# Performance work log

Hardware: AMD Instinct MI355X
Metric: run time of the kernel (lower is better)

The kernel has to match this reference:

```python
import jax, jax.numpy as jnp
import numpy as np

N = 100000
E = 3200000
F_IN = 256
HID = 128


def _dconv_k1(x_cat, w, b):
    # torch_geometric_temporal DConv with K=1:
    # H = X @ W[0,0] + X @ W[1,0] + b   (no graph propagation for K=1)
    return x_cat @ (w[0, 0] + w[1, 0]) + b


def _dcrnn_cell(x, h, wz, bz, wr, br, wh, bh):
    xh = jnp.concatenate([x, h], axis=1)
    z = jax.nn.sigmoid(_dconv_k1(xh, wz, bz))
    r = jax.nn.sigmoid(_dconv_k1(xh, wr, br))
    xrh = jnp.concatenate([x, r * h], axis=1)
    h_tilde = jnp.tanh(_dconv_k1(xrh, wh, bh))
    return z * h + (1.0 - z) * h_tilde


def setup_inputs() -> dict:
    key = jax.random.key(0)
    ks = jax.random.split(key, 16)

    def gw(k, shape):
        fan_in = shape[-2]
        return jax.random.normal(k, shape, dtype=jnp.float32) / np.sqrt(fan_in)

    inp = {
        "x": jax.random.normal(ks[0], (N, F_IN), dtype=jnp.float32),
        "edge_index": jax.random.randint(ks[1], (2, E), 0, N, dtype=jnp.int64 if jax.config.jax_enable_x64 else jnp.int32),
        "edge_weight": jax.random.uniform(ks[2], (E,), dtype=jnp.float32),
        "w_z1": gw(ks[3], (2, 1, F_IN + HID, HID)), "b_z1": jnp.zeros((HID,), jnp.float32),
        "w_r1": gw(ks[4], (2, 1, F_IN + HID, HID)), "b_r1": jnp.zeros((HID,), jnp.float32),
        "w_h1": gw(ks[5], (2, 1, F_IN + HID, HID)), "b_h1": jnp.zeros((HID,), jnp.float32),
        "w_z2": gw(ks[6], (2, 1, HID + HID // 2, HID // 2)), "b_z2": jnp.zeros((HID // 2,), jnp.float32),
        "w_r2": gw(ks[7], (2, 1, HID + HID // 2, HID // 2)), "b_r2": jnp.zeros((HID // 2,), jnp.float32),
        "w_h2": gw(ks[8], (2, 1, HID + HID // 2, HID // 2)), "b_h2": jnp.zeros((HID // 2,), jnp.float32),
        "w_lin1": gw(ks[9], (HID // 2, 16)), "b_lin1": jnp.zeros((16,), jnp.float32),
        "w_lin2": gw(ks[10], (16, 1)), "b_lin2": jnp.zeros((1,), jnp.float32),
    }
    return inp


def reference(x, edge_index, edge_weight,
              w_z1, b_z1, w_r1, b_r1, w_h1, b_h1,
              w_z2, b_z2, w_r2, b_r2, w_h2, b_h2,
              w_lin1, b_lin1, w_lin2, b_lin2):
    # edge_index / edge_weight are unused in the K=1 DConv math (faithful to tgt source).
    h0 = jnp.zeros((x.shape[0], w_z1.shape[-1]), x.dtype)
    h = _dcrnn_cell(x, h0, w_z1, b_z1, w_r1, b_r1, w_h1, b_h1)
    h = jax.nn.relu(h)
    h0b = jnp.zeros((x.shape[0], w_z2.shape[-1]), x.dtype)
    h = _dcrnn_cell(h, h0b, w_z2, b_z2, w_r2, b_r2, w_h2, b_h2)
    h = jax.nn.relu(h)
    # Dropout(0.2) is identity at inference
    h = jax.nn.relu(h @ w_lin1 + b_lin1)
    return h @ w_lin2 + b_lin2
```

## Files before the change

kernel.cpp:

```cpp
#include <hip/hip_runtime.h>

typedef _Float16 f16;
typedef _Float16 f16x4 __attribute__((ext_vector_type(4)));
typedef _Float16 f16x8 __attribute__((ext_vector_type(8)));
typedef float    f32x4 __attribute__((ext_vector_type(4)));

#define N_ROWS 100000
#define RT 1563
#define TPB 256
#define LSX 264
#define LSH1 136
#define LSH2 72

#define W1F_OFF 0
#define W1F_BYTES (256 * 256 * 2)
#define W2F_OFF W1F_BYTES

#define ARENA 33792
#define H1S 0
#define H2S 17408

__global__ void prep_w(const float* __restrict__ wz1, const float* __restrict__ wh1,
                       const float* __restrict__ wz2, const float* __restrict__ wh2,
                       f16* __restrict__ W1F, f16* __restrict__ W2F) {
    const int b = blockIdx.x, tid = threadIdx.x;
    if (b < 32) {
        int idx = b * 256 + tid;
        int l = idx & 63, itm = idx >> 6;
        int it = itm & 7, M = itm >> 3;
        int ln = l & 15, q = l >> 4;
        int col = M * 16 + ln;
        int k0 = it * 32 + q * 8;
        const float* w = (col < 128) ? wz1 : wh1;
        int cc = col & 127;
        f16x8 v;
#pragma unroll
        for (int j = 0; j < 8; ++j) {
            int k = k0 + j;
            v[j] = (f16)(w[k * 128 + cc] + w[384 * 128 + k * 128 + cc]);
        }
        *(f16x8*)&W1F[idx * 8] = v;
    } else {
        int idx = (b - 32) * 256 + tid;
        if (idx >= 2048) return;
        int l = idx & 63, tkc = idx >> 6;
        int kc = tkc & 3, t = tkc >> 2;
        int ln = l & 15, q = l >> 4;
        int col = (t < 4) ? (16 * t + ln) : (64 + 16 * (t - 4) + ln);
        int k0 = kc * 32 + q * 8;
        const float* w = (col < 64) ? wz2 : wh2;
        int cc = col & 63;
        f16x8 v;
#pragma unroll
        for (int j = 0; j < 8; ++j) {
            int k = k0 + j;
            v[j] = (f16)(w[k * 64 + cc] + w[192 * 64 + k * 64 + cc]);
        }
        *(f16x8*)&W2F[idx * 8] = v;
    }
}

__device__ __forceinline__ float gate(float zp, float hp) {
    float e2h = __expf(2.0f * fminf(hp, 15.0f));
    float ez  = __expf(zp);
    float r   = __builtin_amdgcn_rcpf((e2h + 1.0f) * (1.0f + ez));
    return fmaxf((e2h - 1.0f) * r, 0.0f);
}

__global__ __launch_bounds__(TPB, 3) void fused(
    const float* __restrict__ x,
    const f16* __restrict__ W1F, const f16* __restrict__ W2F,
    const float* __restrict__ bz1, const float* __restrict__ bh1,
    const float* __restrict__ bz2, const float* __restrict__ bh2,
    const float* __restrict__ wl1, const float* __restrict__ bl1,
    const float* __restrict__ wl2, const float* __restrict__ bl2,
    float* __restrict__ out)
{
    __shared__ __align__(16) char arena[ARENA];
    const int tid = threadIdx.x, lane = tid & 63, wave = tid >> 6;
    const int ln = lane & 15, quad = lane >> 4;
    const int r0 = blockIdx.x * 64;

    const int xr = tid >> 2, xcg = tid & 3;
    int gxr = r0 + xr; if (gxr >= N_ROWS) gxr = N_ROWS - 1;
    const float* xp = x + (size_t)gxr * 256 + (xcg << 3);

    f16* Xs = (f16*)arena;

    const f16* wb0 = W1F + (size_t)wave * 4096 + (size_t)lane * 8;

    f32x4 acc[4][4];
#pragma unroll
    for (int a = 0; a < 4; ++a)
#pragma unroll
        for (int b = 0; b < 4; ++b) acc[a][b] = (f32x4){0.f, 0.f, 0.f, 0.f};

    f32x4 pa = __builtin_nontemporal_load((const f32x4*)(xp));
    f32x4 pb = __builtin_nontemporal_load((const f32x4*)(xp + 4));
    f16x8 afc[4], afn[4];
#pragma unroll
    for (int mi = 0; mi < 4; ++mi)
        afc[mi] = *(const f16x8*)(wb0 + mi * 16384);

#pragma unroll
    for (int s = 0; s < 8; ++s) {
        *(f16x8*)&Xs[xr * LSX + s * 32 + (xcg << 3)] =
            (f16x8){(f16)pa[0],(f16)pa[1],(f16)pa[2],(f16)pa[3],
                    (f16)pb[0],(f16)pb[1],(f16)pb[2],(f16)pb[3]};
        asm volatile("s_waitcnt lgkmcnt(0)" ::: "memory");
        __builtin_amdgcn_s_barrier();
        asm volatile("" ::: "memory");
        if (s < 7) {
            pa = __builtin_nontemporal_load((const f32x4*)(xp + (s + 1) * 32));
            pb = __builtin_nontemporal_load((const f32x4*)(xp + (s + 1) * 32 + 4));
#pragma unroll
            for (int mi = 0; mi < 4; ++mi)
                afn[mi] = *(const f16x8*)(wb0 + mi * 16384 + (s + 1) * 512);
        }
        f16x8 bf[4];
#pragma unroll
        for (int nt = 0; nt < 4; ++nt)
            bf[nt] = *(const f16x8*)&Xs[(16 * nt + ln) * LSX + s * 32 + quad * 8];
#pragma unroll
        for (int nt = 0; nt < 4; ++nt)
#pragma unroll
            for (int mi = 0; mi < 4; ++mi)
                acc[mi][nt] = __builtin_amdgcn_mfma_f32_16x16x32_f16(afc[mi], bf[nt], acc[mi][nt], 0, 0, 0);
#pragma unroll
        for (int mi = 0; mi < 4; ++mi) afc[mi] = afn[mi];
    }
    __syncthreads();

    f16x8 w2f[2][4];
#pragma unroll
    for (int kc = 0; kc < 4; ++kc) {
        w2f[0][kc] = *(const f16x8*)(W2F + ((size_t)((wave    ) * 4 + kc) * 64 + lane) * 8);
        w2f[1][kc] = *(const f16x8*)(W2F + ((size_t)((wave + 4) * 4 + kc) * 64 + lane) * 8);
    }

    f16* h1s = (f16*)(arena + H1S);
#pragma unroll
    for (int zi = 0; zi < 2; ++zi) {
        const int jg0 = 16 * (wave + 4 * zi) + (quad << 2);
        const float4 zb = *(const float4*)(bz1 + jg0);
        const float4 hb = *(const float4*)(bh1 + jg0);
#pragma unroll
        for (int nt = 0; nt < 4; ++nt) {
            const int row = 16 * nt + ln;
            f16x4 pk;
#pragma unroll
            for (int i = 0; i < 4; ++i)
                pk[i] = (f16)gate(acc[zi][nt][i] + (&zb.x)[i],
                                  acc[zi + 2][nt][i] + (&hb.x)[i]);
            *(f16x4*)&h1s[row * LSH1 + jg0] = pk;
        }
    }
    __syncthreads();

    f32x4 acc2[2][4];
#pragma unroll
    for (int a = 0; a < 2; ++a)
#pragma unroll
        for (int b = 0; b < 4; ++b) acc2[a][b] = (f32x4){0.f, 0.f, 0.f, 0.f};
#pragma unroll
    for (int kc = 0; kc < 4; ++kc) {
        f16x8 bf[4];
#pragma unroll
        for (int nt = 0; nt < 4; ++nt)
            bf[nt] = *(const f16x8*)&h1s[(16 * nt + ln) * LSH1 + kc * 32 + quad * 8];
#pragma unroll
        for (int m = 0; m < 2; ++m)
#pragma unroll
            for (int nt = 0; nt < 4; ++nt)
                acc2[m][nt] = __builtin_amdgcn_mfma_f32_16x16x32_f16(w2f[m][kc], bf[nt], acc2[m][nt], 0, 0, 0);
    }

    f16* h2s = (f16*)(arena + H2S);
    {
        const int jg0 = 16 * wave + (quad << 2);
        const float4 zb = *(const float4*)(bz2 + jg0);
        const float4 hb = *(const float4*)(bh2 + jg0);
#pragma unroll
        for (int nt = 0; nt < 4; ++nt) {
            const int row = 16 * nt + ln;
            f16x4 pk;
#pragma unroll
            for (int i = 0; i < 4; ++i)
                pk[i] = (f16)gate(acc2[0][nt][i] + (&zb.x)[i],
                                  acc2[1][nt][i] + (&hb.x)[i]);
            *(f16x4*)&h2s[row * LSH2 + jg0] = pk;
        }
    }
    __syncthreads();

    const float blv = bl1[ln], wlv = wl2[ln], bl2v = bl2[0];
    f16x8 bfr[2];
#pragma unroll
    for (int kc = 0; kc < 2; ++kc)
#pragma unroll
        for (int j = 0; j < 8; ++j)
            bfr[kc][j] = (f16)wl1[(32 * kc + 8 * quad + j) * 16 + ln];

    f32x4 acc3 = (f32x4){0.f, 0.f, 0.f, 0.f};
#pragma unroll
    for (int kc = 0; kc < 2; ++kc) {
        f16x8 af = *(const f16x8*)&h2s[(16 * wave + ln) * LSH2 + kc * 32 + quad * 8];
        acc3 = __builtin_amdgcn_mfma_f32_16x16x32_f16(af, bfr[kc], acc3, 0, 0, 0);
    }
#pragma unroll
    for (int i = 0; i < 4; ++i) {
        float v = fmaxf(acc3[i] + blv, 0.0f) * wlv;
        v += __shfl_xor(v, 1);
        v += __shfl_xor(v, 2);
        v += __shfl_xor(v, 4);
        v += __shfl_xor(v, 8);
        if (ln == 0) {
            const int row = r0 + 16 * wave + (quad << 2) + i;
            if (row < N_ROWS) out[row] = v + bl2v;
        }
    }
}

extern "C" void kernel_launch(void* const* d_in, const int* in_sizes, int n_in,
                              void* d_out, int out_size, void* d_ws, size_t ws_size,
                              hipStream_t stream) {
    const float* x   = (const float*)d_in[0];
    const float* wz1 = (const float*)d_in[3];
    const float* bz1 = (const float*)d_in[4];
    const float* wh1 = (const float*)d_in[7];
    const float* bh1 = (const float*)d_in[8];
    const float* wz2 = (const float*)d_in[9];
    const float* bz2 = (const float*)d_in[10];
    const float* wh2 = (const float*)d_in[13];
    const float* bh2 = (const float*)d_in[14];
    const float* wl1 = (const float*)d_in[15];
    const float* bl1 = (const float*)d_in[16];
    const float* wl2 = (const float*)d_in[17];
    const float* bl2 = (const float*)d_in[18];

    char* ws = (char*)d_ws;
    f16* W1F = (f16*)(ws + W1F_OFF);
    f16* W2F = (f16*)(ws + W2F_OFF);
    float* out = (float*)d_out;

    prep_w<<<40, 256, 0, stream>>>(wz1, wh1, wz2, wh2, W1F, W2F);
    fused<<<RT, TPB, 0, stream>>>(x, W1F, W2F, bz1, bh1, bz2, bh2,
                                  wl1, bl1, wl2, bl2, out);
}
```

Baseline: 218.7 us.

## Make fused kernel persistent with double-buffered x tiles prefetched during GEMM

```diff
diff --git a/kernel.cpp b/kernel.cpp
--- a/kernel.cpp
+++ b/kernel.cpp
@@ -6,7 +6,8 @@
 typedef float    f32x4 __attribute__((ext_vector_type(4)));
 
 #define N_ROWS 100000
-#define RT 1563
+#define NTILE 1563
+#define GRID 521
 #define TPB 256
 #define LSX 264
 #define LSH1 136
@@ -16,9 +17,10 @@
 #define W1F_BYTES (256 * 256 * 2)
 #define W2F_OFF W1F_BYTES
 
-#define ARENA 33792
-#define H1S 0
-#define H2S 17408
+#define XHALF 33792
+#define ARENA (2 * XHALF)
+#define H1OFF 0
+#define H2OFF 17408
 
 __global__ void prep_w(const float* __restrict__ wz1, const float* __restrict__ wh1,
                        const float* __restrict__ wz2, const float* __restrict__ wh2,
@@ -67,7 +69,7 @@
     return fmaxf((e2h - 1.0f) * r, 0.0f);
 }
 
-__global__ __launch_bounds__(TPB, 3) void fused(
+__global__ __launch_bounds__(TPB, 2) void fused(
     const float* __restrict__ x,
     const f16* __restrict__ W1F, const f16* __restrict__ W2F,
     const float* __restrict__ bz1, const float* __restrict__ bh1,
@@ -79,57 +81,10 @@
     __shared__ __align__(16) char arena[ARENA];
     const int tid = threadIdx.x, lane = tid & 63, wave = tid >> 6;
     const int ln = lane & 15, quad = lane >> 4;
-    const int r0 = blockIdx.x * 64;
 
     const int xr = tid >> 2, xcg = tid & 3;
-    int gxr = r0 + xr; if (gxr >= N_ROWS) gxr = N_ROWS - 1;
-    const float* xp = x + (size_t)gxr * 256 + (xcg << 3);
-
-    f16* Xs = (f16*)arena;
 
     const f16* wb0 = W1F + (size_t)wave * 4096 + (size_t)lane * 8;
-
-    f32x4 acc[4][4];
-#pragma unroll
-    for (int a = 0; a < 4; ++a)
-#pragma unroll
-        for (int b = 0; b < 4; ++b) acc[a][b] = (f32x4){0.f, 0.f, 0.f, 0.f};
-
-    f32x4 pa = __builtin_nontemporal_load((const f32x4*)(xp));
-    f32x4 pb = __builtin_nontemporal_load((const f32x4*)(xp + 4));
-    f16x8 afc[4], afn[4];
-#pragma unroll
-    for (int mi = 0; mi < 4; ++mi)
-        afc[mi] = *(const f16x8*)(wb0 + mi * 16384);
-
-#pragma unroll
-    for (int s = 0; s < 8; ++s) {
-        *(f16x8*)&Xs[xr * LSX + s * 32 + (xcg << 3)] =
-            (f16x8){(f16)pa[0],(f16)pa[1],(f16)pa[2],(f16)pa[3],
-                    (f16)pb[0],(f16)pb[1],(f16)pb[2],(f16)pb[3]};
-        asm volatile("s_waitcnt lgkmcnt(0)" ::: "memory");
-        __builtin_amdgcn_s_barrier();
-        asm volatile("" ::: "memory");
-        if (s < 7) {
-            pa = __builtin_nontemporal_load((const f32x4*)(xp + (s + 1) * 32));
-            pb = __builtin_nontemporal_load((const f32x4*)(xp + (s + 1) * 32 + 4));
-#pragma unroll
-            for (int mi = 0; mi < 4; ++mi)
-                afn[mi] = *(const f16x8*)(wb0 + mi * 16384 + (s + 1) * 512);
-        }
-        f16x8 bf[4];
-#pragma unroll
-        for (int nt = 0; nt < 4; ++nt)
-            bf[nt] = *(const f16x8*)&Xs[(16 * nt + ln) * LSX + s * 32 + quad * 8];
-#pragma unroll
-        for (int nt = 0; nt < 4; ++nt)
-#pragma unroll
-            for (int mi = 0; mi < 4; ++mi)
-                acc[mi][nt] = __builtin_amdgcn_mfma_f32_16x16x32_f16(afc[mi], bf[nt], acc[mi][nt], 0, 0, 0);
-#pragma unroll
-        for (int mi = 0; mi < 4; ++mi) afc[mi] = afn[mi];
-    }
-    __syncthreads();
 
     f16x8 w2f[2][4];
 #pragma unroll
@@ -137,62 +92,6 @@
         w2f[0][kc] = *(const f16x8*)(W2F + ((size_t)((wave    ) * 4 + kc) * 64 + lane) * 8);
         w2f[1][kc] = *(const f16x8*)(W2F + ((size_t)((wave + 4) * 4 + kc) * 64 + lane) * 8);
     }
-
-    f16* h1s = (f16*)(arena + H1S);
-#pragma unroll
-    for (int zi = 0; zi < 2; ++zi) {
-        const int jg0 = 16 * (wave + 4 * zi) + (quad << 2);
-        const float4 zb = *(const float4*)(bz1 + jg0);
-        const float4 hb = *(const float4*)(bh1 + jg0);
-#pragma unroll
-        for (int nt = 0; nt < 4; ++nt) {
-            const int row = 16 * nt + ln;
-            f16x4 pk;
-#pragma unroll
-            for (int i = 0; i < 4; ++i)
-                pk[i] = (f16)gate(acc[zi][nt][i] + (&zb.x)[i],
-                                  acc[zi + 2][nt][i] + (&hb.x)[i]);
-            *(f16x4*)&h1s[row * LSH1 + jg0] = pk;
-        }
-    }
-    __syncthreads();
-
-    f32x4 acc2[2][4];
-#pragma unroll
-    for (int a = 0; a < 2; ++a)
-#pragma unroll
-        for (int b = 0; b < 4; ++b) acc2[a][b] = (f32x4){0.f, 0.f, 0.f, 0.f};
-#pragma unroll
-    for (int kc = 0; kc < 4; ++kc) {
-        f16x8 bf[4];
-#pragma unroll
-        for (int nt = 0; nt < 4; ++nt)
-            bf[nt] = *(const f16x8*)&h1s[(16 * nt + ln) * LSH1 + kc * 32 + quad * 8];
-#pragma unroll
-        for (int m = 0; m < 2; ++m)
-#pragma unroll
-            for (int nt = 0; nt < 4; ++nt)
-                acc2[m][nt] = __builtin_amdgcn_mfma_f32_16x16x32_f16(w2f[m][kc], bf[nt], acc2[m][nt], 0, 0, 0);
-    }
-
-    f16* h2s = (f16*)(arena + H2S);
-    {
-        const int jg0 = 16 * wave + (quad << 2);
-        const float4 zb = *(const float4*)(bz2 + jg0);
-        const float4 hb = *(const float4*)(bh2 + jg0);
-#pragma unroll
-        for (int nt = 0; nt < 4; ++nt) {
-            const int row = 16 * nt + ln;
-            f16x4 pk;
-#pragma unroll
-            for (int i = 0; i < 4; ++i)
-                pk[i] = (f16)gate(acc2[0][nt][i] + (&zb.x)[i],
-                                  acc2[1][nt][i] + (&hb.x)[i]);
-            *(f16x4*)&h2s[row * LSH2 + jg0] = pk;
-        }
-    }
-    __syncthreads();
-
     const float blv = bl1[ln], wlv = wl2[ln], bl2v = bl2[0];
     f16x8 bfr[2];
 #pragma unroll
@@ -201,23 +100,163 @@
         for (int j = 0; j < 8; ++j)
             bfr[kc][j] = (f16)wl1[(32 * kc + 8 * quad + j) * 16 + ln];
 
-    f32x4 acc3 = (f32x4){0.f, 0.f, 0.f, 0.f};
-#pragma unroll
-    for (int kc = 0; kc < 2; ++kc) {
-        f16x8 af = *(const f16x8*)&h2s[(16 * wave + ln) * LSH2 + kc * 32 + quad * 8];
-        acc3 = __builtin_amdgcn_mfma_f32_16x16x32_f16(af, bfr[kc], acc3, 0, 0, 0);
-    }
-#pragma unroll
-    for (int i = 0; i < 4; ++i) {
-        float v = fmaxf(acc3[i] + blv, 0.0f) * wlv;
-        v += __shfl_xor(v, 1);
-        v += __shfl_xor(v, 2);
-        v += __shfl_xor(v, 4);
-        v += __shfl_xor(v, 8);
-        if (ln == 0) {
-            const int row = r0 + 16 * wave + (quad << 2) + i;
-            if (row < N_ROWS) out[row] = v + bl2v;
-        }
+    auto xrow = [&](int tt) {
+        int r = tt * 64 + xr; if (r >= N_ROWS) r = N_ROWS - 1;
+        return x + (size_t)r * 256 + (xcg << 3);
+    };
+
+    {
+        const float* xp = xrow(blockIdx.x);
+        f16* b0 = (f16*)arena;
+#pragma unroll
+        for (int half = 0; half < 2; ++half) {
+            f32x4 a[4], c[4];
+#pragma unroll
+            for (int kc = 0; kc < 4; ++kc) {
+                a[kc] = __builtin_nontemporal_load((const f32x4*)(xp + (half * 4 + kc) * 32));
+                c[kc] = __builtin_nontemporal_load((const f32x4*)(xp + (half * 4 + kc) * 32 + 4));
+            }
+#pragma unroll
+            for (int kc = 0; kc < 4; ++kc)
+                *(f16x8*)&b0[xr * LSX + (half * 4 + kc) * 32 + (xcg << 3)] =
+                    (f16x8){(f16)a[kc][0],(f16)a[kc][1],(f16)a[kc][2],(f16)a[kc][3],
+                            (f16)c[kc][0],(f16)c[kc][1],(f16)c[kc][2],(f16)c[kc][3]};
+        }
+    }
+    __syncthreads();
+
+#pragma unroll 1
+    for (int t = 0; t < 3; ++t) {
+        const int tt = blockIdx.x + GRID * t;
+        f16* cur = (f16*)(arena + (t & 1) * XHALF);
+        f16* nxt = (f16*)(arena + ((t + 1) & 1) * XHALF);
+        const bool hn = (t < 2);
+        const float* xpn = hn ? xrow(tt + GRID) : (const float*)nullptr;
+
+        f32x4 pa[3], pb[3];
+        if (hn) {
+#pragma unroll
+            for (int d = 0; d < 3; ++d) {
+                pa[d] = __builtin_nontemporal_load((const f32x4*)(xpn + d * 32));
+                pb[d] = __builtin_nontemporal_load((const f32x4*)(xpn + d * 32 + 4));
+            }
+        }
+
+        f32x4 acc[4][4];
+#pragma unroll
+        for (int a = 0; a < 4; ++a)
+#pragma unroll
+            for (int b = 0; b < 4; ++b) acc[a][b] = (f32x4){0.f, 0.f, 0.f, 0.f};
+
+        f16x8 afc[4], afn[4];
+#pragma unroll
+        for (int mi = 0; mi < 4; ++mi)
+            afc[mi] = *(const f16x8*)(wb0 + mi * 16384);
+
+#pragma unroll
+        for (int s = 0; s < 8; ++s) {
+            if (s < 7) {
+#pragma unroll
+                for (int mi = 0; mi < 4; ++mi)
+                    afn[mi] = *(const f16x8*)(wb0 + mi * 16384 + (s + 1) * 512);
+            }
+            if (hn) {
+                const int sl = s % 3;
+                *(f16x8*)&nxt[xr * LSX + s * 32 + (xcg << 3)] =
+                    (f16x8){(f16)pa[sl][0],(f16)pa[sl][1],(f16)pa[sl][2],(f16)pa[sl][3],
+                            (f16)pb[sl][0],(f16)pb[sl][1],(f16)pb[sl][2],(f16)pb[sl][3]};
+                if (s + 3 < 8) {
+                    pa[sl] = __builtin_nontemporal_load((const f32x4*)(xpn + (s + 3) * 32));
+                    pb[sl] = __builtin_nontemporal_load((const f32x4*)(xpn + (s + 3) * 32 + 4));
+                }
+            }
+            f16x8 bf[4];
+#pragma unroll
+            for (int nt = 0; nt < 4; ++nt)
+                bf[nt] = *(const f16x8*)&cur[(16 * nt + ln) * LSX + s * 32 + quad * 8];
+#pragma unroll
+            for (int nt = 0; nt < 4; ++nt)
+#pragma unroll
+                for (int mi = 0; mi < 4; ++mi)
+                    acc[mi][nt] = __builtin_amdgcn_mfma_f32_16x16x32_f16(afc[mi], bf[nt], acc[mi][nt], 0, 0, 0);
+#pragma unroll
+            for (int mi = 0; mi < 4; ++mi) afc[mi] = afn[mi];
+        }
+        __syncthreads();
+
+        f16* h1s = (f16*)((char*)cur + H1OFF);
+        f16* h2s = (f16*)((char*)cur + H2OFF);
+#pragma unroll
+        for (int zi = 0; zi < 2; ++zi) {
+            const int jg0 = 16 * (wave + 4 * zi) + (quad << 2);
+            const float4 zb = *(const float4*)(bz1 + jg0);
+            const float4 hb = *(const float4*)(bh1 + jg0);
+#pragma unroll
+            for (int nt = 0; nt < 4; ++nt) {
+                const int row = 16 * nt + ln;
+                f16x4 pk;
+#pragma unroll
+                for (int i = 0; i < 4; ++i)
+                    pk[i] = (f16)gate(acc[zi][nt][i] + (&zb.x)[i],
+                                      acc[zi + 2][nt][i] + (&hb.x)[i]);
+                *(f16x4*)&h1s[row * LSH1 + jg0] = pk;
+            }
+        }
+        __syncthreads();
+
+        f32x4 acc2[2][4];
+#pragma unroll
+        for (int a = 0; a < 2; ++a)
+#pragma unroll
+            for (int b = 0; b < 4; ++b) acc2[a][b] = (f32x4){0.f, 0.f, 0.f, 0.f};
+#pragma unroll
+        for (int kc = 0; kc < 4; ++kc) {
+            f16x8 bf[4];
+#pragma unroll
+            for (int nt = 0; nt < 4; ++nt)
+                bf[nt] = *(const f16x8*)&h1s[(16 * nt + ln) * LSH1 + kc * 32 + quad * 8];
+#pragma unroll
+            for (int m = 0; m < 2; ++m)
+#pragma unroll
+                for (int nt = 0; nt < 4; ++nt)
+                    acc2[m][nt] = __builtin_amdgcn_mfma_f32_16x16x32_f16(w2f[m][kc], bf[nt], acc2[m][nt], 0, 0, 0);
+        }
+        {
+            const int jg0 = 16 * wave + (quad << 2);
+            const float4 zb = *(const float4*)(bz2 + jg0);
+            const float4 hb = *(const float4*)(bh2 + jg0);
+#pragma unroll
+            for (int nt = 0; nt < 4; ++nt) {
+                const int row = 16 * nt + ln;
+                f16x4 pk;
+#pragma unroll
+                for (int i = 0; i < 4; ++i)
+                    pk[i] = (f16)gate(acc2[0][nt][i] + (&zb.x)[i],
+                                      acc2[1][nt][i] + (&hb.x)[i]);
+                *(f16x4*)&h2s[row * LSH2 + jg0] = pk;
+            }
+        }
+        __syncthreads();
+
+        f32x4 acc3 = (f32x4){0.f, 0.f, 0.f, 0.f};
+#pragma unroll
+        for (int kc = 0; kc < 2; ++kc) {
+            f16x8 af = *(const f16x8*)&h2s[(16 * wave + ln) * LSH2 + kc * 32 + quad * 8];
+            acc3 = __builtin_amdgcn_mfma_f32_16x16x32_f16(af, bfr[kc], acc3, 0, 0, 0);
+        }
+#pragma unroll
+        for (int i = 0; i < 4; ++i) {
+            float v = fmaxf(acc3[i] + blv, 0.0f) * wlv;
+            v += __shfl_xor(v, 1);
+            v += __shfl_xor(v, 2);
+            v += __shfl_xor(v, 4);
+            v += __shfl_xor(v, 8);
+            if (ln == 0) {
+                const int row = tt * 64 + 16 * wave + (quad << 2) + i;
+                if (row < N_ROWS) out[row] = v + bl2v;
+            }
+        }
+        __syncthreads();
     }
 }
 
@@ -244,6 +283,6 @@
     float* out = (float*)d_out;
 
     prep_w<<<40, 256, 0, stream>>>(wz1, wh1, wz2, wh2, W1F, W2F);
-    fused<<<RT, TPB, 0, stream>>>(x, W1F, W2F, bz1, bh1, bz2, bh2,
-                                  wl1, bl1, wl2, bl2, out);
-}
+    fused<<<GRID, TPB, 0, stream>>>(x, W1F, W2F, bz1, bh1, bz2, bh2,
+                                    wl1, bl1, wl2, bl2, out);
+}
```

Result: slower. 268.3 us (+22.7%).
